# Kernel optimization log

Hardware: AMD Instinct MI355X
Metric: run time of the kernel (lower is better)

Reference implementation:

```python
import jax, jax.numpy as jnp
import numpy as np

D_ATTN = 2048
D_STATE = 64
SHIFT_FRAC = 0.5
LN_EPS = 1e-5


def setup_inputs() -> dict:
    key = jax.random.key(0)
    ks = jax.random.split(key, 8)
    B, T = 8, 2048
    s_attn = 1.0 / np.sqrt(D_ATTN)
    s_state = 1.0 / np.sqrt(D_STATE)
    x = jax.random.normal(ks[0], (B, T, D_ATTN), jnp.float32)
    W_key = jax.random.normal(ks[1], (D_STATE, D_ATTN), jnp.float32) * s_attn
    W_value = jax.random.normal(ks[2], (D_STATE, D_ATTN), jnp.float32) * s_attn
    W_output = jax.random.normal(ks[3], (D_ATTN, D_STATE), jnp.float32) * s_state
    W_shift = jax.random.normal(ks[4], (D_ATTN, D_ATTN), jnp.float32) * s_attn
    gate = jnp.ones((D_ATTN,), jnp.float32)
    # negative decay log so w = exp(time_decay) in (e^-1, 1): stable over T=2048 steps
    time_decay = -jax.random.uniform(ks[5], (D_STATE,), jnp.float32, 0.05, 1.0)
    time_first = jax.random.normal(ks[6], (D_STATE,), jnp.float32) * 0.1
    ln_gamma = jnp.ones((D_ATTN,), jnp.float32)
    ln_beta = jnp.zeros((D_ATTN,), jnp.float32)
    return dict(x=x, W_key=W_key, W_value=W_value, W_output=W_output,
                W_shift=W_shift, gate=gate, time_decay=time_decay,
                time_first=time_first, ln_gamma=ln_gamma, ln_beta=ln_beta)


def reference(x, W_key, W_value, W_output, W_shift, gate, time_decay,
              time_first, ln_gamma, ln_beta):
    B, T, D = x.shape
    # token shift: cat([x[:, s:], x[:, :-s]], dim=1) == roll(x, -s, axis=1)
    shift_len = max(1, int(T * SHIFT_FRAC))
    x_cat = jnp.roll(x, -shift_len, axis=1)
    g = jax.nn.sigmoid(gate)
    x_shift = jnp.einsum('btd,ed->bte', x_cat, W_shift) * g + x * (1.0 - g)
    # LayerNorm over last dim
    mu = jnp.mean(x_shift, axis=-1, keepdims=True)
    var = jnp.var(x_shift, axis=-1, keepdims=True)
    x_norm = (x_shift - mu) * jax.lax.rsqrt(var + LN_EPS) * ln_gamma + ln_beta
    k = jnp.einsum('btd,sd->bts', x_norm, W_key)    # (B,T,Ds)
    v = jnp.einsum('btd,sd->bts', x_norm, W_value)  # (B,T,Ds)
    w = jnp.exp(time_decay)                          # (Ds,)
    u = jnp.exp(time_first)                          # (Ds,)
    wkv = jnp.exp(-u * jax.nn.sigmoid(k)) * v        # (B,T,Ds)
    # linear recurrence: state_t = w * state_{t-1} + wkv_t
    def step(state, wkv_t):
        state = state * w + wkv_t
        return state, state
    init = jnp.zeros((B, k.shape[-1]), x.dtype)
    last_state, states = jax.lax.scan(step, init, jnp.swapaxes(wkv, 0, 1))
    states = jnp.swapaxes(states, 0, 1)              # (B,T,Ds)
    # per-step output projection == single batched GEMM over stacked states
    output = jnp.einsum('bts,ds->btd', states, W_output)  # (B,T,D)
    # dropout in eval mode is identity; last_state is detached in original
    return output, jax.lax.stop_gradient(last_state)
```

## Files before the change

### kernel.cpp

```cpp
#include <hip/hip_runtime.h>
#include <stdint.h>

constexpr int kD  = 2048;
constexpr int kDS = 64;
constexpr int kNT = 2048;
constexpr int kM  = 8 * kNT;
constexpr int kOutElems = kM * kD;

typedef __attribute__((ext_vector_type(8))) short short8;
typedef __attribute__((ext_vector_type(8))) unsigned short bfu8;
typedef __attribute__((ext_vector_type(4))) unsigned short bfu4;
typedef __attribute__((ext_vector_type(4))) float f32x4;

__device__ __forceinline__ unsigned short f2bf(float f) {
  unsigned int u = __float_as_uint(f);
  return (unsigned short)((u + 0x7FFFu + ((u >> 16) & 1u)) >> 16);
}
__device__ __forceinline__ float bf2f(unsigned short b) {
  return __uint_as_float(((unsigned int)b) << 16);
}

__device__ __forceinline__ void gload16(const void* g, void* l) {
  __builtin_amdgcn_global_load_lds((__attribute__((address_space(1))) void*)g,
                                   (__attribute__((address_space(3))) void*)l,
                                   16, 0, 0);
}

__global__ void k_cvt(const float* __restrict__ src, unsigned short* __restrict__ dst, int n8) {
  int i8 = blockIdx.x * 256 + threadIdx.x;
  if (i8 >= n8) return;
  const f32x4* s = (const f32x4*)(src + (size_t)i8 * 8);
  f32x4 v0 = s[0], v1 = s[1];
  bfu8 o;
  o[0] = f2bf(v0[0]); o[1] = f2bf(v0[1]); o[2] = f2bf(v0[2]); o[3] = f2bf(v0[3]);
  o[4] = f2bf(v1[0]); o[5] = f2bf(v1[1]); o[6] = f2bf(v1[2]); o[7] = f2bf(v1[3]);
  *(bfu8*)(dst + (size_t)i8 * 8) = o;
}

__global__ void k_cvt_kv(const float* __restrict__ wk, const float* __restrict__ wv,
                         unsigned short* __restrict__ dst) {
  int i8 = blockIdx.x * 256 + threadIdx.x;
  int r = i8 >> 8;
  int dcol = (i8 & 255) << 3;
  int s = r >> 1;
  const float* src = (r & 1) ? wv : wk;
  const f32x4* p = (const f32x4*)(src + (size_t)s * kD + dcol);
  f32x4 v0 = p[0], v1 = p[1];
  bfu8 o;
  o[0] = f2bf(v0[0]); o[1] = f2bf(v0[1]); o[2] = f2bf(v0[2]); o[3] = f2bf(v0[3]);
  o[4] = f2bf(v1[0]); o[5] = f2bf(v1[1]); o[6] = f2bf(v1[2]); o[7] = f2bf(v1[3]);
  *(bfu8*)(dst + (size_t)i8 * 8) = o;
}

#define MM(x,y,z) __builtin_amdgcn_mfma_f32_16x16x32_bf16(x,y,z,0,0,0)
#define BAR __builtin_amdgcn_s_barrier()
#define WAITV_(N) asm volatile("s_waitcnt vmcnt(" #N ")" ::: "memory")
#define WAITV(N) WAITV_(N)
#define WAITL asm volatile("s_waitcnt lgkmcnt(0)")

#define STAGEA_TO(BUF,H,Q,KT) gload16(aS + (size_t)(((H)*64+(Q)*128)*2048) + (KT), \
                                      smem + (BUF)*32768 + ((H)*64+(Q)*128)*64 + ldsAst)
#define STAGEB_TO(BUF,H,Q,KT) gload16(bS + (size_t)(((H)*32+(Q)*128)*2048) + (KT), \
                                      smem + (BUF)*32768 + 16384 + (H)*2048 + (Q)*8192 + ldsBst)

#define RDA(CUR,H,MF,KS) (*(const short8*)(smem + (CUR)*32768 + ardb + (H)*4096 + (MF)*1024 + colrd##KS))
#define RDB(CUR,H,NF,KS) (*(const short8*)(smem + (CUR)*32768 + 16384 + brdb + (H)*2048 + (NF)*1024 + colrd##KS))

#define RD_A(CUR,H) \
  a[0][0]=RDA(CUR,H,0,0); a[0][1]=RDA(CUR,H,0,1); \
  a[1][0]=RDA(CUR,H,1,0); a[1][1]=RDA(CUR,H,1,1); \
  a[2][0]=RDA(CUR,H,2,0); a[2][1]=RDA(CUR,H,2,1); \
  a[3][0]=RDA(CUR,H,3,0); a[3][1]=RDA(CUR,H,3,1)
#define RD_B(CUR,H,BV) \
  BV[0][0]=RDB(CUR,H,0,0); BV[0][1]=RDB(CUR,H,0,1); \
  BV[1][0]=RDB(CUR,H,1,0); BV[1][1]=RDB(CUR,H,1,1)

#define MF16(MH, B, NB) \
  __builtin_amdgcn_s_setprio(1); \
  acc[(MH)*4+0][(NB)+0] = MM(a[0][0], B[0][0], acc[(MH)*4+0][(NB)+0]); \
  acc[(MH)*4+0][(NB)+0] = MM(a[0][1], B[0][1], acc[(MH)*4+0][(NB)+0]); \
  acc[(MH)*4+0][(NB)+1] = MM(a[0][0], B[1][0], acc[(MH)*4+0][(NB)+1]); \
  acc[(MH)*4+0][(NB)+1] = MM(a[0][1], B[1][1], acc[(MH)*4+0][(NB)+1]); \
  acc[(MH)*4+1][(NB)+0] = MM(a[1][0], B[0][0], acc[(MH)*4+1][(NB)+0]); \
  acc[(MH)*4+1][(NB)+0] = MM(a[1][1], B[0][1], acc[(MH)*4+1][(NB)+0]); \
  acc[(MH)*4+1][(NB)+1] = MM(a[1][0], B[1][0], acc[(MH)*4+1][(NB)+1]); \
  acc[(MH)*4+1][(NB)+1] = MM(a[1][1], B[1][1], acc[(MH)*4+1][(NB)+1]); \
  acc[(MH)*4+2][(NB)+0] = MM(a[2][0], B[0][0], acc[(MH)*4+2][(NB)+0]); \
  acc[(MH)*4+2][(NB)+0] = MM(a[2][1], B[0][1], acc[(MH)*4+2][(NB)+0]); \
  acc[(MH)*4+2][(NB)+1] = MM(a[2][0], B[1][0], acc[(MH)*4+2][(NB)+1]); \
  acc[(MH)*4+2][(NB)+1] = MM(a[2][1], B[1][1], acc[(MH)*4+2][(NB)+1]); \
  acc[(MH)*4+3][(NB)+0] = MM(a[3][0], B[0][0], acc[(MH)*4+3][(NB)+0]); \
  acc[(MH)*4+3][(NB)+0] = MM(a[3][1], B[0][1], acc[(MH)*4+3][(NB)+0]); \
  acc[(MH)*4+3][(NB)+1] = MM(a[3][0], B[1][0], acc[(MH)*4+3][(NB)+1]); \
  acc[(MH)*4+3][(NB)+1] = MM(a[3][1], B[1][1], acc[(MH)*4+3][(NB)+1]); \
  __builtin_amdgcn_s_setprio(0)

#define TILE2(CUR, KT1, KT2, S0, S123, VA, VB, DOVE, VE) \
  RD_A(CUR,0); RD_B(CUR,0,b0); \
  if (S0) { STAGEA_TO((CUR)^1, 1, 0, KT1); STAGEA_TO((CUR)^1, 1, 1, KT1); } \
  BAR; WAITL; MF16(0, b0, 0); WAITV(VA); BAR; \
  RD_B(CUR,1,b1); \
  if (S123) { STAGEA_TO(CUR, 0, 0, KT2); STAGEA_TO(CUR, 0, 1, KT2); } \
  BAR; WAITL; MF16(0, b1, 2); WAITV(VB); BAR; \
  RD_A(CUR,1); \
  if (S123) { STAGEB_TO(CUR, 0, 0, KT2); STAGEB_TO(CUR, 0, 1, KT2); } \
  BAR; WAITL; MF16(1, b0, 0); BAR; \
  if (S123) { STAGEB_TO(CUR, 1, 0, KT2); STAGEB_TO(CUR, 1, 1, KT2); } \
  MF16(1, b1, 2); if (DOVE) { WAITV(VE); } BAR

__global__ __launch_bounds__(512, 2)
void k_gemm_shift8(const unsigned short* __restrict__ A,
                   const unsigned short* __restrict__ Bw,
                   const float* __restrict__ gate,
                   unsigned short* __restrict__ out) {
  __shared__ __align__(16) unsigned char smem_raw[131072];
  unsigned short* smem = (unsigned short*)smem_raw;

  const int tid = threadIdx.x;
  const int lane = tid & 63;
  const int w = tid >> 6;
  const int wr = w >> 2, wc = w & 3;
  const int lr = lane & 15, lq = lane >> 4;
  const int bid = blockIdx.x;
  const int nblk = bid & 7, mblk = bid >> 3;
  const int m0 = mblk * 256, n0 = nblk * 256;

  const int r0 = tid >> 3;
  const int colel = ((tid & 7) * 8) ^ (((tid >> 3) & 7) << 3);
  const unsigned short* aS = A + (size_t)((m0 ^ 1024) + r0) * 2048 + colel;
  const unsigned short* bS = Bw + (size_t)(n0 + ((tid >> 8) << 6) + (r0 & 31)) * 2048 + colel;
  const int ldsAst = tid * 8;
  const int ldsBst = ((tid >> 8) << 12) + (tid & 255) * 8;

  const int ardb = (wr * 128 + lr) * 64;
  const int brdb = (wc * 64 + lr) * 64;
  const int colrd0 = (lq * 8) ^ ((lr & 7) << 3);
  const int colrd1 = (32 + lq * 8) ^ ((lr & 7) << 3);

  short8 a[4][2], b0[2][2], b1[2][2];
  f32x4 acc[8][4] = {};

  STAGEA_TO(0,0,0,0); STAGEA_TO(0,0,1,0);
  STAGEB_TO(0,0,0,0); STAGEB_TO(0,0,1,0);
  STAGEB_TO(0,1,0,0); STAGEB_TO(0,1,1,0);
  STAGEA_TO(0,1,0,0); STAGEA_TO(0,1,1,0);
  STAGEA_TO(1,0,0,64); STAGEA_TO(1,0,1,64);
  STAGEB_TO(1,0,0,64); STAGEB_TO(1,0,1,64);
  STAGEB_TO(1,1,0,64); STAGEB_TO(1,1,1,64);
  WAITV(10); BAR;

  int k1 = 64, k2 = 128;
  for (int j = 0; j < 15; ++j) {
    TILE2(0, k1, k2, 1, 1, 10, 10, 1, 10); k1 += 64; k2 += 64;
    TILE2(1, k1, k2, 1, 1, 10, 10, 1, 10); k1 += 64; k2 += 64;
  }
  TILE2(0, k1, k2, 1, 0, 10, 8, 1, 4);
  TILE2(1, 0, 0, 0, 0, 2, 0, 0, 0);

  float* cbuf = (float*)smem_raw;
#pragma unroll
  for (int q = 0; q < 4; ++q) {
    __syncthreads();
    if (wr == (q >> 1)) {
#pragma unroll
      for (int mm = 0; mm < 4; ++mm) {
#pragma unroll
        for (int nf = 0; nf < 4; ++nf) {
#pragma unroll
          for (int i = 0; i < 4; ++i) {
            int rl = mm * 16 + lq * 4 + i;
            int cl = wc * 64 + nf * 16 + lr;
            cbuf[rl * 260 + cl] = acc[(q & 1) * 4 + mm][nf][i];
          }
        }
      }
    }
    __syncthreads();
#pragma unroll
    for (int it = 0; it < 4; ++it) {
      int idx = tid + it * 512;
      int rl = idx >> 5, cb = (idx & 31) * 8;
      int gr = m0 + q * 64 + rl, gc = n0 + cb;
      f32x4 c0 = *(const f32x4*)&cbuf[rl * 260 + cb];
      f32x4 c1 = *(const f32x4*)&cbuf[rl * 260 + cb + 4];
      f32x4 g0 = *(const f32x4*)&gate[gc];
      f32x4 g1 = *(const f32x4*)&gate[gc + 4];
      bfu8 xv = *(const bfu8*)(A + (size_t)gr * 2048 + gc);
      bfu8 o;
#pragma unroll
      for (int jj = 0; jj < 4; ++jj) {
        float g = 1.f / (1.f + __expf(-g0[jj]));
        o[jj] = f2bf(c0[jj] * g + bf2f(xv[jj]) * (1.f - g));
        float h = 1.f / (1.f + __expf(-g1[jj]));
        o[jj + 4] = f2bf(c1[jj] * h + bf2f(xv[jj + 4]) * (1.f - h));
      }
      *(bfu8*)(out + (size_t)gr * 2048 + gc) = o;
    }
  }
}

__launch_bounds__(256)
__global__ void k_ln(const unsigned short* __restrict__ xs, const float* __restrict__ gamma,
                     const float* __restrict__ beta, unsigned short* __restrict__ xn) {
  int m = blockIdx.x;
  int tid = threadIdx.x;
  bfu8 v = *(const bfu8*)(xs + (size_t)m * kD + tid * 8);
  float f[8];
#pragma unroll
  for (int j = 0; j < 8; ++j) f[j] = bf2f(v[j]);
  float s = 0.f, q = 0.f;
#pragma unroll
  for (int j = 0; j < 8; ++j) { s += f[j]; q += f[j] * f[j]; }
#pragma unroll
  for (int d = 1; d < 64; d <<= 1) { s += __shfl_xor(s, d); q += __shfl_xor(q, d); }
  __shared__ float ss[4], qq[4];
  if ((tid & 63) == 0) { ss[tid >> 6] = s; qq[tid >> 6] = q; }
  __syncthreads();
  s = ss[0] + ss[1] + ss[2] + ss[3];
  q = qq[0] + qq[1] + qq[2] + qq[3];
  float mean = s * (1.f / kD);
  float var = q * (1.f / kD) - mean * mean;
  float rstd = rsqrtf(var + 1e-5f);
  int d0 = tid * 8;
  bfu8 o;
#pragma unroll
  for (int j = 0; j < 8; ++j) {
    float g = gamma[d0 + j], b = beta[d0 + j];
    o[j] = f2bf((f[j] - mean) * rstd * g + b);
  }
  *(bfu8*)(xn + (size_t)m * kD + d0) = o;
}

__launch_bounds__(256, 2)
__global__ void k_gemm_kv(const unsigned short* __restrict__ A,
                          const unsigned short* __restrict__ Bw,
                          const float* __restrict__ tfirst,
                          float* __restrict__ wkv) {
  __shared__ __align__(16) unsigned short As[32 * 32];
  __shared__ __align__(16) unsigned short Bs[128 * 32];
  const int tid = threadIdx.x;
  const int lane = tid & 63;
  const int wcv = tid >> 6;
  const int m0 = blockIdx.x * 32;
  const int lr = lane & 15, lk = (lane >> 4) << 3;
  const int c1 = tid, c2 = tid + 256;

  const unsigned short* ga = A + (size_t)(m0 + (tid >> 2)) * kD + ((tid & 3) << 3);
  const unsigned short* gb0 = Bw + (size_t)(c1 >> 2) * kD + ((c1 & 3) << 3);
  const unsigned short* gb1 = Bw + (size_t)(c2 >> 2) * kD + ((c2 & 3) << 3);
  unsigned short* la = As + tid * 8;
  unsigned short* lb0 = Bs + c1 * 8;
  unsigned short* lb1 = Bs + c2 * 8;

  f32x4 acc[2][2] = {};

  for (int kt = 0; kt < kD; kt += 32) {
    __syncthreads();
    if (tid < 128) gload16(ga + kt, la);
    gload16(gb0 + kt, lb0);
    gload16(gb1 + kt, lb1);
    __syncthreads();
    short8 af[2], bf[2];
#pragma unroll
    for (int mf = 0; mf < 2; ++mf)
      af[mf] = *(const short8*)&As[(mf * 16 + lr) * 32 + lk];
#pragma unroll
    for (int nf = 0; nf < 2; ++nf)
      bf[nf] = *(const short8*)&Bs[(wcv * 32 + nf * 16 + lr) * 32 + lk];
#pragma unroll
    for (int mf = 0; mf < 2; ++mf)
#pragma unroll
      for (int nf = 0; nf < 2; ++nf)
        acc[mf][nf] = __builtin_amdgcn_mfma_f32_16x16x32_bf16(af[mf], bf[nf], acc[mf][nf], 0, 0, 0);
  }

  const int fq = lane >> 4, fr = lane & 15;
#pragma unroll
  for (int mf = 0; mf < 2; ++mf) {
#pragma unroll
    for (int nf = 0; nf < 2; ++nf) {
      int c = wcv * 32 + nf * 16 + fr;
#pragma unroll
      for (int i = 0; i < 4; ++i) {
        int r = m0 + mf * 16 + fq * 4 + i;
        float val = acc[mf][nf][i];
        float other = __shfl_xor(val, 1);
        if (!(c & 1)) {
          int s = c >> 1;
          float sk = 1.f / (1.f + expf(-val));
          float u = expf(tfirst[s]);
          wkv[(size_t)r * kDS + s] = expf(-u * sk) * other;
        }
      }
    }
  }
}

__global__ void k_scan(const float* __restrict__ wkv, const float* __restrict__ tdec,
                       float* __restrict__ states, float* __restrict__ last_state) {
  int chunk = blockIdx.x;
  int b = blockIdx.y;
  int s = threadIdx.x;
  float w = expf(tdec[s]);
  int t1 = chunk * 64;
  int warm = t1 < 256 ? t1 : 256;
  const float* base = wkv + (size_t)b * kNT * kDS + s;
  float* sbase = states + (size_t)b * kNT * kDS + s;
  float st = 0.f;
#pragma unroll 4
  for (int t = t1 - warm; t < t1; ++t) st = fmaf(st, w, base[(size_t)t * kDS]);
#pragma unroll 4
  for (int t = t1; t < t1 + 64; ++t) {
    st = fmaf(st, w, base[(size_t)t * kDS]);
    sbase[(size_t)t * kDS] = st;
  }
  if (chunk == 31) last_state[b * kDS + s] = st;
}

__launch_bounds__(256, 3)
__global__ void k_out_gemm(const float* __restrict__ states, const float* __restrict__ Wo,
                           float* __restrict__ out) {
  __shared__ float St[64 * 68];
  __shared__ float Wt[64 * 132];
  const int m0 = blockIdx.y * 64;
  const int n0 = blockIdx.x * 128;
  const int tid = threadIdx.x;
#pragma unroll
  for (int it = 0; it < 16; ++it) {
    int idx = tid + it * 256;
    int r = idx >> 6, s = idx & 63;
    St[s * 68 + r] = states[(size_t)(m0 + r) * kDS + s];
  }
#pragma unroll
  for (int it = 0; it < 32; ++it) {
    int idx = tid + it * 256;
    int dl = idx >> 6, s = idx & 63;
    Wt[s * 132 + dl] = Wo[(size_t)(n0 + dl) * kDS + s];
  }
  __syncthreads();
  const int pr = tid & 15, pc = tid >> 4;
  float acc[4][8] = {};
  for (int s = 0; s < 64; ++s) {
    f32x4 sv = *(const f32x4*)&St[s * 68 + pr * 4];
    f32x4 w0 = *(const f32x4*)&Wt[s * 132 + pc * 8];
    f32x4 w1 = *(const f32x4*)&Wt[s * 132 + pc * 8 + 4];
#pragma unroll
    for (int i = 0; i < 4; ++i) {
      float aa = sv[i];
#pragma unroll
      for (int j = 0; j < 4; ++j) {
        acc[i][j] = fmaf(aa, w0[j], acc[i][j]);
        acc[i][j + 4] = fmaf(aa, w1[j], acc[i][j + 4]);
      }
    }
  }
#pragma unroll
  for (int i = 0; i < 4; ++i) {
    int r = m0 + pr * 4 + i;
    f32x4 o0 = {acc[i][0], acc[i][1], acc[i][2], acc[i][3]};
    f32x4 o1 = {acc[i][4], acc[i][5], acc[i][6], acc[i][7]};
    *(f32x4*)&out[(size_t)r * kD + n0 + pc * 8] = o0;
    *(f32x4*)&out[(size_t)r * kD + n0 + pc * 8 + 4] = o1;
  }
}

extern "C" void kernel_launch(void* const* d_in, const int* in_sizes, int n_in,
                              void* d_out, int out_size, void* d_ws, size_t ws_size,
                              hipStream_t stream) {
  const float* x    = (const float*)d_in[0];
  const float* Wk   = (const float*)d_in[1];
  const float* Wv   = (const float*)d_in[2];
  const float* Wo   = (const float*)d_in[3];
  const float* Wsh  = (const float*)d_in[4];
  const float* gate = (const float*)d_in[5];
  const float* tdec = (const float*)d_in[6];
  const float* tfir = (const float*)d_in[7];
  const float* lng  = (const float*)d_in[8];
  const float* lnb  = (const float*)d_in[9];
  float* out = (float*)d_out;
  char* ws = (char*)d_ws;

  unsigned short* xbf   = (unsigned short*)(ws);
  unsigned short* wshbf = (unsigned short*)(ws + 67108864);
  unsigned short* wkvbf = (unsigned short*)(ws + 75497472);
  float* wkvf           = (float*)(ws + 76021760);
  float* statesf        = (float*)(ws + 80216064);

  k_cvt<<<16384, 256, 0, stream>>>(x, xbf, 4194304);
  k_cvt<<<2048, 256, 0, stream>>>(Wsh, wshbf, 524288);
  k_cvt_kv<<<128, 256, 0, stream>>>(Wk, Wv, wkvbf);

  k_gemm_shift8<<<512, 512, 0, stream>>>(xbf, wshbf, gate, (unsigned short*)out);
  k_ln<<<16384, 256, 0, stream>>>((const unsigned short*)out, lng, lnb, xbf);
  k_gemm_kv<<<512, 256, 0, stream>>>(xbf, wkvbf, tfir, wkvf);
  k_scan<<<dim3(32, 8), 64, 0, stream>>>(wkvf, tdec, statesf, out + kOutElems);
  k_out_gemm<<<dim3(16, 256), 256, 0, stream>>>(statesf, Wo, out);
}
```

Measured before the change: 318.9 us.

## Restructure GEMM main loop into software-pipelined phases with early LDS prefetch

```diff
diff --git a/kernel.cpp b/kernel.cpp
--- a/kernel.cpp
+++ b/kernel.cpp
@@ -57,6 +57,7 @@
 #define WAITV_(N) asm volatile("s_waitcnt vmcnt(" #N ")" ::: "memory")
 #define WAITV(N) WAITV_(N)
 #define WAITL asm volatile("s_waitcnt lgkmcnt(0)")
+#define NOWV (void)0
 
 #define STAGEA_TO(BUF,H,Q,KT) gload16(aS + (size_t)(((H)*64+(Q)*128)*2048) + (KT), \
                                       smem + (BUF)*32768 + ((H)*64+(Q)*128)*64 + ldsAst)
@@ -78,35 +79,45 @@
 #define MF16(MH, B, NB) \
   __builtin_amdgcn_s_setprio(1); \
   acc[(MH)*4+0][(NB)+0] = MM(a[0][0], B[0][0], acc[(MH)*4+0][(NB)+0]); \
+  acc[(MH)*4+0][(NB)+1] = MM(a[0][0], B[1][0], acc[(MH)*4+0][(NB)+1]); \
+  acc[(MH)*4+1][(NB)+0] = MM(a[1][0], B[0][0], acc[(MH)*4+1][(NB)+0]); \
+  acc[(MH)*4+1][(NB)+1] = MM(a[1][0], B[1][0], acc[(MH)*4+1][(NB)+1]); \
+  acc[(MH)*4+2][(NB)+0] = MM(a[2][0], B[0][0], acc[(MH)*4+2][(NB)+0]); \
+  acc[(MH)*4+2][(NB)+1] = MM(a[2][0], B[1][0], acc[(MH)*4+2][(NB)+1]); \
+  acc[(MH)*4+3][(NB)+0] = MM(a[3][0], B[0][0], acc[(MH)*4+3][(NB)+0]); \
+  acc[(MH)*4+3][(NB)+1] = MM(a[3][0], B[1][0], acc[(MH)*4+3][(NB)+1]); \
   acc[(MH)*4+0][(NB)+0] = MM(a[0][1], B[0][1], acc[(MH)*4+0][(NB)+0]); \
-  acc[(MH)*4+0][(NB)+1] = MM(a[0][0], B[1][0], acc[(MH)*4+0][(NB)+1]); \
   acc[(MH)*4+0][(NB)+1] = MM(a[0][1], B[1][1], acc[(MH)*4+0][(NB)+1]); \
-  acc[(MH)*4+1][(NB)+0] = MM(a[1][0], B[0][0], acc[(MH)*4+1][(NB)+0]); \
   acc[(MH)*4+1][(NB)+0] = MM(a[1][1], B[0][1], acc[(MH)*4+1][(NB)+0]); \
-  acc[(MH)*4+1][(NB)+1] = MM(a[1][0], B[1][0], acc[(MH)*4+1][(NB)+1]); \
   acc[(MH)*4+1][(NB)+1] = MM(a[1][1], B[1][1], acc[(MH)*4+1][(NB)+1]); \
-  acc[(MH)*4+2][(NB)+0] = MM(a[2][0], B[0][0], acc[(MH)*4+2][(NB)+0]); \
   acc[(MH)*4+2][(NB)+0] = MM(a[2][1], B[0][1], acc[(MH)*4+2][(NB)+0]); \
-  acc[(MH)*4+2][(NB)+1] = MM(a[2][0], B[1][0], acc[(MH)*4+2][(NB)+1]); \
   acc[(MH)*4+2][(NB)+1] = MM(a[2][1], B[1][1], acc[(MH)*4+2][(NB)+1]); \
-  acc[(MH)*4+3][(NB)+0] = MM(a[3][0], B[0][0], acc[(MH)*4+3][(NB)+0]); \
   acc[(MH)*4+3][(NB)+0] = MM(a[3][1], B[0][1], acc[(MH)*4+3][(NB)+0]); \
-  acc[(MH)*4+3][(NB)+1] = MM(a[3][0], B[1][0], acc[(MH)*4+3][(NB)+1]); \
   acc[(MH)*4+3][(NB)+1] = MM(a[3][1], B[1][1], acc[(MH)*4+3][(NB)+1]); \
   __builtin_amdgcn_s_setprio(0)
 
-#define TILE2(CUR, KT1, KT2, S0, S123, VA, VB, DOVE, VE) \
-  RD_A(CUR,0); RD_B(CUR,0,b0); \
-  if (S0) { STAGEA_TO((CUR)^1, 1, 0, KT1); STAGEA_TO((CUR)^1, 1, 1, KT1); } \
-  BAR; WAITL; MF16(0, b0, 0); WAITV(VA); BAR; \
+#define PH0(CUR, S, KA1, WV) \
+  BAR; WAITL; MF16(0, b0, 0); \
   RD_B(CUR,1,b1); \
-  if (S123) { STAGEA_TO(CUR, 0, 0, KT2); STAGEA_TO(CUR, 0, 1, KT2); } \
-  BAR; WAITL; MF16(0, b1, 2); WAITV(VB); BAR; \
+  if (S) { STAGEA_TO((CUR)^1, 1, 0, KA1); STAGEA_TO((CUR)^1, 1, 1, KA1); } \
+  WV
+
+#define PH1(CUR, S, KT2, WV) \
+  BAR; WAITL; MF16(0, b1, 2); \
   RD_A(CUR,1); \
-  if (S123) { STAGEB_TO(CUR, 0, 0, KT2); STAGEB_TO(CUR, 0, 1, KT2); } \
-  BAR; WAITL; MF16(1, b0, 0); BAR; \
-  if (S123) { STAGEB_TO(CUR, 1, 0, KT2); STAGEB_TO(CUR, 1, 1, KT2); } \
-  MF16(1, b1, 2); if (DOVE) { WAITV(VE); } BAR
+  if (S) { STAGEA_TO(CUR, 0, 0, KT2); STAGEA_TO(CUR, 0, 1, KT2); } \
+  WV
+
+#define PH2(CUR, S, KT2, WV) \
+  BAR; WAITL; MF16(1, b0, 0); \
+  if (S) { STAGEB_TO(CUR, 0, 0, KT2); STAGEB_TO(CUR, 0, 1, KT2); } \
+  WV
+
+#define PH3(CUR, RDN, S, KT2, WV) \
+  BAR; WAITL; MF16(1, b1, 2); \
+  if (RDN) { RD_A((CUR)^1,0); RD_B((CUR)^1,0,b0); } \
+  if (S) { STAGEB_TO(CUR, 1, 0, KT2); STAGEB_TO(CUR, 1, 1, KT2); } \
+  WV
 
 __global__ __launch_bounds__(512, 2)
 void k_gemm_shift8(const unsigned short* __restrict__ A,
@@ -147,15 +158,22 @@
   STAGEA_TO(1,0,0,64); STAGEA_TO(1,0,1,64);
   STAGEB_TO(1,0,0,64); STAGEB_TO(1,0,1,64);
   STAGEB_TO(1,1,0,64); STAGEB_TO(1,1,1,64);
-  WAITV(10); BAR;
-
-  int k1 = 64, k2 = 128;
+  WAITV(6); BAR;
+  RD_A(0,0); RD_B(0,0,b0);
+
+  int ka1 = 64, kt2 = 128;
   for (int j = 0; j < 15; ++j) {
-    TILE2(0, k1, k2, 1, 1, 10, 10, 1, 10); k1 += 64; k2 += 64;
-    TILE2(1, k1, k2, 1, 1, 10, 10, 1, 10); k1 += 64; k2 += 64;
-  }
-  TILE2(0, k1, k2, 1, 0, 10, 8, 1, 4);
-  TILE2(1, 0, 0, 0, 0, 2, 0, 0, 0);
+    PH0(0, 1, ka1, WAITV(8)); PH1(0, 1, kt2, WAITV(8));
+    PH2(0, 1, kt2, WAITV(8)); PH3(0, 1, 1, kt2, WAITV(8));
+    ka1 += 64; kt2 += 64;
+    PH0(1, 1, ka1, WAITV(8)); PH1(1, 1, kt2, WAITV(8));
+    PH2(1, 1, kt2, WAITV(8)); PH3(1, 1, 1, kt2, WAITV(8));
+    ka1 += 64; kt2 += 64;
+  }
+  PH0(0, 1, 1984, WAITV(8)); PH1(0, 0, 0, NOWV);
+  PH2(0, 0, 0, WAITV(4));    PH3(0, 1, 0, 0, WAITV(2));
+  PH0(1, 0, 0, WAITV(0));    PH1(1, 0, 0, NOWV);
+  PH2(1, 0, 0, NOWV);        PH3(1, 0, 0, 0, NOWV);
 
   float* cbuf = (float*)smem_raw;
 #pragma unroll
```

New measurement: 312.6 us. 1.02x faster.
